# Kernel optimization log

Hardware: AMD Instinct MI355X
Metric: run time of the kernel (lower is better)

Reference implementation:

```python
import jax, jax.numpy as jnp
import numpy as np

C = 256
D = C // 8  # query/key channels


def setup_inputs() -> dict:
    key = jax.random.key(0)
    ks = jax.random.split(key, 7)
    x = jax.random.normal(ks[0], (4, C, 64, 64), dtype=jnp.float32)
    s1 = 1.0 / np.sqrt(C)
    w1 = jax.random.normal(ks[1], (D, C), dtype=jnp.float32) * s1
    b1 = jax.random.normal(ks[2], (D,), dtype=jnp.float32) * 0.01
    w2 = jax.random.normal(ks[3], (D, C), dtype=jnp.float32) * s1
    b2 = jax.random.normal(ks[4], (D,), dtype=jnp.float32) * 0.01
    w3 = jax.random.normal(ks[5], (C, C), dtype=jnp.float32) * s1
    b3 = jax.random.normal(ks[6], (C,), dtype=jnp.float32) * 0.01
    return {"x": x, "w1": w1, "b1": b1, "w2": w2, "b2": b2, "w3": w3, "b3": b3}


def reference(x, w1, b1, w2, b2, w3, b3):
    B, Cc, W, H = x.shape
    N = W * H
    xf = x.reshape(B, Cc, N)  # [B, C, N] flattened spatial
    # 1x1 convs are per-pixel linear maps over channels
    q = jnp.einsum('dc,bcn->bnd', w1, xf) + b1  # [B, N, D]
    k = jnp.einsum('dc,bcn->bdn', w2, xf) + b2[:, None]  # [B, D, N]
    v = jnp.einsum('oc,bcn->bon', w3, xf) + b3[:, None]  # [B, C, N]
    energy = jnp.einsum('bnd,bdm->bnm', q, k)  # [B, N, N]
    attn = jax.nn.softmax(energy, axis=-1)
    out = jnp.einsum('bcm,bnm->bcn', v, attn)  # bmm(V, attn^T)
    out = out.reshape(B, Cc, W, H) + x
    return out
```

## Files before the change

kernel.cpp:

```cpp
#include <hip/hip_runtime.h>
#include <hip/hip_fp16.h>

typedef _Float16 half8 __attribute__((ext_vector_type(8)));
typedef _Float16 half2v __attribute__((ext_vector_type(2)));
typedef float f32x16 __attribute__((ext_vector_type(16)));
typedef float f32x4v __attribute__((ext_vector_type(4)));

#define MFMA16(A, B, C) __builtin_amdgcn_mfma_f32_32x32x16_f16((A), (B), (C), 0, 0, 0)

__device__ __forceinline__ f32x16 fzero16() {
  f32x16 z;
#pragma unroll
  for (int i = 0; i < 16; ++i) z[i] = 0.0f;
  return z;
}

struct HiLo { _Float16 hi, lo; };
__device__ __forceinline__ HiLo split1(float f) {
  HiLo r;
  r.hi = (_Float16)f;
  r.lo = (_Float16)(f - (float)r.hi);
  return r;
}

__global__ __launch_bounds__(256) void wprep_kernel(
    const float* __restrict__ w1, const float* __restrict__ w2,
    const float* __restrict__ w3,
    _Float16* __restrict__ w1p, _Float16* __restrict__ w2p,
    _Float16* __restrict__ w3p)
{
  const int t = threadIdx.x;
  const int blk = blockIdx.x;
  if (blk < 8) {
    const int cot = blk;
    for (int e = t; e < 8192; e += 256) {
      const int j = e & 7, l = (e >> 3) & 63, cs = e >> 9;
      const int lr = l & 31, h = l >> 5;
      const int row = cot * 32 + lr;
      const int col = cs * 16 + 4 * h + (j & 3) + 8 * (j >> 2);
      const HiLo s = split1(w3[row * 256 + col]);
      const int idx = ((cot * 16 + cs) * 64 + l) * 8 + j;
      w3p[idx] = s.hi;
      w3p[65536 + idx] = s.lo;
    }
  } else {
    for (int e = t; e < 8192; e += 256) {
      const int j = e & 7, l = (e >> 3) & 63, cs = e >> 9;
      const int lr = l & 31, h = l >> 5;
      const int col = cs * 16 + 4 * h + (j & 3) + 8 * (j >> 2);
      const HiLo s1 = split1(w1[lr * 256 + col]);
      const HiLo s2 = split1(w2[lr * 256 + col]);
      const int idx = (cs * 64 + l) * 8 + j;
      w1p[idx] = s1.hi; w1p[8192 + idx] = s1.lo;
      w2p[idx] = s2.hi; w2p[8192 + idx] = s2.lo;
    }
  }
}

__global__ __launch_bounds__(256) void qk_proj_kernel(
    const float* __restrict__ x,
    const _Float16* __restrict__ w1p, const float* __restrict__ b1,
    const _Float16* __restrict__ w2p, const float* __restrict__ b2,
    _Float16* __restrict__ qb, _Float16* __restrict__ kb)
{
  __shared__ f32x4v red[4][2][4][64];
  const int t = threadIdx.x, w = t >> 6, l = t & 63;
  const int lr = l & 31, h = l >> 5;
  const int b = blockIdx.x >> 7;
  const int rt = blockIdx.x & 127;
  const float* xb = x + (size_t)b * 256 * 4096 + rt * 32 + lr;

  f32x16 accq = fzero16(), acck = fzero16();

  for (int cs = w * 4; cs < w * 4 + 4; ++cs) {
    const int c0 = cs * 16 + 4 * h;
    half8 xh, xl;
#pragma unroll
    for (int j = 0; j < 8; ++j) {
      const int c = c0 + (j & 3) + 8 * (j >> 2);
      const HiLo s = split1(xb[(size_t)c * 4096]);
      xh[j] = s.hi; xl[j] = s.lo;
    }
    const half8 w1h = *(const half8*)&w1p[(cs * 64 + l) * 8];
    const half8 w1l = *(const half8*)&w1p[8192 + (cs * 64 + l) * 8];
    const half8 w2h = *(const half8*)&w2p[(cs * 64 + l) * 8];
    const half8 w2l = *(const half8*)&w2p[8192 + (cs * 64 + l) * 8];
    accq = MFMA16(w1h, xh, accq);
    accq = MFMA16(w1h, xl, accq);
    accq = MFMA16(w1l, xh, accq);
    acck = MFMA16(w2h, xh, acck);
    acck = MFMA16(w2h, xl, acck);
    acck = MFMA16(w2l, xh, acck);
  }

#pragma unroll
  for (int i4 = 0; i4 < 4; ++i4) {
    f32x4v q4, k4;
#pragma unroll
    for (int c = 0; c < 4; ++c) { q4[c] = accq[4 * i4 + c]; k4[c] = acck[4 * i4 + c]; }
    red[w][0][i4][l] = q4;
    red[w][1][i4][l] = k4;
  }
  __syncthreads();
  if (w < 2) {
    _Float16* dst = (w == 0) ? qb : kb;
    const float* bias = (w == 0) ? b1 : b2;
    f32x16 tot;
#pragma unroll
    for (int i4 = 0; i4 < 4; ++i4) {
      f32x4v v = red[0][w][i4][l];
      v += red[1][w][i4][l];
      v += red[2][w][i4][l];
      v += red[3][w][i4][l];
#pragma unroll
      for (int c = 0; c < 4; ++c) tot[4 * i4 + c] = v[c];
    }
#pragma unroll
    for (int ds = 0; ds < 2; ++ds) {
      half8 ph;
#pragma unroll
      for (int j = 0; j < 8; ++j) {
        const int d = 16 * ds + 4 * h + (j & 3) + 8 * (j >> 2);
        ph[j] = (_Float16)(tot[8 * ds + j] + bias[d]);
      }
      *(half8*)&dst[((((size_t)b * 128 + rt) * 2 + ds) * 64 + l) * 8] = ph;
    }
  }
}

__global__ __launch_bounds__(256) void v_proj_kernel(
    const float* __restrict__ x, const _Float16* __restrict__ w3p,
    const float* __restrict__ b3, _Float16* __restrict__ vb)
{
  const int t = threadIdx.x, w = t >> 6, l = t & 63;
  const int lr = l & 31, h = l >> 5;
  const int b = blockIdx.x >> 7;
  const int nt = blockIdx.x & 127;
  const float* xb = x + (size_t)b * 256 * 4096 + nt * 32 + lr;
  const int cot0 = w * 2, cot1 = w * 2 + 1;

  f32x16 acc0 = fzero16(), acc1 = fzero16();

  for (int cs = 0; cs < 16; ++cs) {
    const int c0 = cs * 16 + 4 * h;
    half8 xh, xl;
#pragma unroll
    for (int j = 0; j < 8; ++j) {
      const int c = c0 + (j & 3) + 8 * (j >> 2);
      const HiLo s = split1(xb[(size_t)c * 4096]);
      xh[j] = s.hi; xl[j] = s.lo;
    }
    const half8 wh0 = *(const half8*)&w3p[((cot0 * 16 + cs) * 64 + l) * 8];
    const half8 wl0 = *(const half8*)&w3p[65536 + ((cot0 * 16 + cs) * 64 + l) * 8];
    const half8 wh1 = *(const half8*)&w3p[((cot1 * 16 + cs) * 64 + l) * 8];
    const half8 wl1 = *(const half8*)&w3p[65536 + ((cot1 * 16 + cs) * 64 + l) * 8];
    acc0 = MFMA16(xh, wh0, acc0);
    acc0 = MFMA16(xl, wh0, acc0);
    acc0 = MFMA16(xh, wl0, acc0);
    acc1 = MFMA16(xh, wh1, acc1);
    acc1 = MFMA16(xl, wh1, acc1);
    acc1 = MFMA16(xh, wl1, acc1);
  }

  const float bv0 = b3[cot0 * 32 + lr];
  const float bv1 = b3[cot1 * 32 + lr];
#pragma unroll
  for (int hfq = 0; hfq < 2; ++hfq) {
    half8 p0, p1;
#pragma unroll
    for (int j = 0; j < 8; ++j) {
      p0[j] = (_Float16)(acc0[8 * hfq + j] + bv0);
      p1[j] = (_Float16)(acc1[8 * hfq + j] + bv1);
    }
    const int ms = nt * 2 + hfq;
    *(half8*)&vb[((((size_t)b * 256 + ms) * 8 + cot0) * 64 + l) * 8] = p0;
    *(half8*)&vb[((((size_t)b * 256 + ms) * 8 + cot1) * 64 + l) * 8] = p1;
  }
}

__global__ __launch_bounds__(512) void rowmax_kernel(
    const _Float16* __restrict__ qb, const _Float16* __restrict__ kb,
    float* __restrict__ Mrow)
{
  __shared__ float red[2][8][32];
  const int t = threadIdx.x, w = t >> 6, l = t & 63;
  const int bid = blockIdx.x;
  const int xcd = bid & 7;
  const int b = xcd >> 1;
  const int sp = ((bid >> 3) << 1) | (xcd & 1);
  const int sl0 = sp * 2, sl1 = sp * 2 + 1;
  const _Float16* qp0 = qb + ((((size_t)b * 128 + sl0) * 2) * 64 + l) * 8;
  const _Float16* qp1 = qb + ((((size_t)b * 128 + sl1) * 2) * 64 + l) * 8;
  const half8 q00 = *(const half8*)qp0;
  const half8 q01 = *(const half8*)(qp0 + 512);
  const half8 q10 = *(const half8*)qp1;
  const half8 q11 = *(const half8*)(qp1 + 512);
  float vm0 = -3.0e38f, vm1 = -3.0e38f;
  for (int mt = w * 16; mt < w * 16 + 16; ++mt) {
    const _Float16* kp = kb + ((((size_t)b * 128 + mt) * 2) * 64 + l) * 8;
    const half8 k0 = *(const half8*)kp;
    const half8 k1 = *(const half8*)(kp + 512);
    f32x16 s0 = fzero16();
    s0 = MFMA16(k0, q00, s0);
    s0 = MFMA16(k1, q01, s0);
    f32x16 s1 = fzero16();
    s1 = MFMA16(k0, q10, s1);
    s1 = MFMA16(k1, q11, s1);
#pragma unroll
    for (int i = 0; i < 16; ++i) {
      vm0 = fmaxf(vm0, s0[i]);
      vm1 = fmaxf(vm1, s1[i]);
    }
  }
  vm0 = fmaxf(vm0, __shfl_xor(vm0, 32));
  vm1 = fmaxf(vm1, __shfl_xor(vm1, 32));
  if (l < 32) { red[0][w][l] = vm0; red[1][w][l] = vm1; }
  __syncthreads();
  if (t < 64) {
    const int slab = t >> 5, r = t & 31;
    float m = red[slab][0][r];
#pragma unroll
    for (int ww = 1; ww < 8; ++ww) m = fmaxf(m, red[slab][ww][r]);
    Mrow[(size_t)b * 4096 + (sp * 2 + slab) * 32 + r] = m;
  }
}

__global__ __launch_bounds__(512, 1) void attn_kernel(
    const _Float16* __restrict__ qb, const _Float16* __restrict__ kb,
    const _Float16* __restrict__ vb, const float* __restrict__ Mrow,
    const float* __restrict__ x, float* __restrict__ out)
{
  __shared__ __align__(16) _Float16 Plds[2][2][2][8][64][8];
  __shared__ float Lred[2][4][32];
  const int t = threadIdx.x, w = t >> 6, l = t & 63;
  const int lr = l & 31, h = l >> 5;
  const int bid = blockIdx.x;
  const int xcd = bid & 7;
  const int b = xcd >> 1;
  const int rg = ((bid >> 3) << 1) | (xcd & 1);
  const int sw = w >> 2;
  const int kq = w & 3;

  const _Float16* kbase = kb + (size_t)b * 131072 + (size_t)l * 8;
  const _Float16* vbase = vb + (size_t)b * 1048576 + (size_t)w * 512 + (size_t)l * 8;

#define KF(kt, ds) (*(const half8*)(kbase + ((size_t)(((kt) * 4 + kq) * 2 + (ds))) * 512))
#define VF(kt, ks) (*(const half8*)(vbase + ((size_t)(((kt) * 8 + (ks)) * 8)) * 512))

  const int rt32q = rg * 2 + sw;
  const _Float16* qp = qb + (((size_t)b * 128 + rt32q) * 2 * 64 + l) * 8;
  const half8 qf0 = *(const half8*)qp;
  const half8 qf1 = *(const half8*)(qp + 512);
  const float LOG2E = 1.44269504088896340736f;
  const float Mr = Mrow[(size_t)b * 4096 + rt32q * 32 + lr];
  const float nM2 = -Mr * LOG2E;

  f32x16 acc0 = fzero16(), acc1 = fzero16();
  float Lacc = 0.f;
  half8 va0[8], va1[8];
  half8 ka0, ka1, kb0_, kb1_;

#define EXPPACK(S, BUF, TI)                                                    \
  {                                                                            \
    float pvv[16];                                                             \
    float ls = 0.f;                                                            \
    _Pragma("unroll") for (int i = 0; i < 16; ++i) {                           \
      pvv[i] = exp2f(fmaf((S)[i], LOG2E, nM2)); ls += pvv[i];                  \
    }                                                                          \
    Lacc += ls;                                                                \
    union { half8 v; half2v h2[4]; } u0, u1;                                   \
    _Pragma("unroll") for (int jj = 0; jj < 4; ++jj) {                         \
      auto a0 = __builtin_amdgcn_cvt_pkrtz(pvv[2 * jj], pvv[2 * jj + 1]);      \
      auto a1 = __builtin_amdgcn_cvt_pkrtz(pvv[8 + 2 * jj], pvv[8 + 2 * jj + 1]); \
      u0.h2[jj] = *(half2v*)&a0;                                               \
      u1.h2[jj] = *(half2v*)&a1;                                               \
    }                                                                          \
    *(half8*)&Plds[BUF][TI][sw][kq * 2 + 0][l][0] = u0.v;                      \
    *(half8*)&Plds[BUF][TI][sw][kq * 2 + 1][l][0] = u1.v;                      \
  }

#define PVC(CB, TI, VA)                                                        \
  {                                                                            \
    __builtin_amdgcn_s_setprio(1);                                             \
    _Pragma("unroll") for (int ks = 0; ks < 8; ++ks) {                         \
      const half8 pb0 = *(const half8*)&Plds[CB][TI][0][ks][l][0];             \
      const half8 pb1 = *(const half8*)&Plds[CB][TI][1][ks][l][0];             \
      acc0 = MFMA16(VA[ks], pb0, acc0);                                        \
      acc1 = MFMA16(VA[ks], pb1, acc1);                                        \
    }                                                                          \
    __builtin_amdgcn_s_setprio(0);                                             \
  }

#pragma unroll
  for (int ks = 0; ks < 8; ++ks) va0[ks] = VF(0, ks);
#pragma unroll
  for (int ks = 0; ks < 8; ++ks) va1[ks] = VF(1, ks);
  {
    const half8 k00 = KF(0, 0), k01 = KF(0, 1);
    f32x16 s = fzero16();
    s = MFMA16(k00, qf0, s);
    s = MFMA16(k01, qf1, s);
    ka0 = KF(2, 0); ka1 = KF(2, 1);
    EXPPACK(s, 0, 0)
  }
  {
    const half8 k10 = KF(1, 0), k11 = KF(1, 1);
    f32x16 s = fzero16();
    s = MFMA16(k10, qf0, s);
    s = MFMA16(k11, qf1, s);
    kb0_ = KF(3, 0); kb1_ = KF(3, 1);
    EXPPACK(s, 0, 1)
  }
  asm volatile("s_waitcnt lgkmcnt(0)" ::: "memory");
  __builtin_amdgcn_s_barrier();
  asm volatile("" ::: "memory");

  for (int P = 0; P < 16; ++P) {
    const int CB = P & 1, PB = CB ^ 1;
    const int p0 = 2 * P + 2, p1 = 2 * P + 3;

    if (p0 < 32) {
      f32x16 s = fzero16();
      s = MFMA16(ka0, qf0, s);
      s = MFMA16(ka1, qf1, s);
      if (p0 + 2 < 32) { ka0 = KF(p0 + 2, 0); ka1 = KF(p0 + 2, 1); }
      EXPPACK(s, PB, 0)
    }
    PVC(CB, 0, va0)
    if (p0 < 32) {
#pragma unroll
      for (int ks = 0; ks < 8; ++ks) va0[ks] = VF(p0, ks);
    }

    if (p1 < 32) {
      f32x16 s = fzero16();
      s = MFMA16(kb0_, qf0, s);
      s = MFMA16(kb1_, qf1, s);
      if (p1 + 2 < 32) { kb0_ = KF(p1 + 2, 0); kb1_ = KF(p1 + 2, 1); }
      EXPPACK(s, PB, 1)
    }
    PVC(CB, 1, va1)
    if (p1 < 32) {
#pragma unroll
      for (int ks = 0; ks < 8; ++ks) va1[ks] = VF(p1, ks);
    }

    asm volatile("s_waitcnt lgkmcnt(0)" ::: "memory");
    __builtin_amdgcn_s_barrier();
    asm volatile("" ::: "memory");
  }
#undef PVC
#undef EXPPACK
#undef KF
#undef VF

  {
    const float l2 = Lacc + __shfl_xor(Lacc, 32);
    if (l < 32) Lred[sw][kq][lr] = l2;
  }
  __syncthreads();
  const float invL0 = 1.0f / (Lred[0][0][lr] + Lred[0][1][lr] + Lred[0][2][lr] + Lred[0][3][lr]);
  const float invL1 = 1.0f / (Lred[1][0][lr] + Lred[1][1][lr] + Lred[1][2][lr] + Lred[1][3][lr]);

  const float* xb = x + (size_t)b * 1048576;
  float* ob = out + (size_t)b * 1048576;
  const int nn0 = rg * 64 + lr;
  const int nn1 = rg * 64 + 32 + lr;
#pragma unroll
  for (int reg = 0; reg < 16; ++reg) {
    const int crel = (reg & 3) + 8 * (reg >> 2) + 4 * h;
    const int cout = w * 32 + crel;
    const size_t o0 = (size_t)cout * 4096 + nn0;
    ob[o0] = acc0[reg] * invL0 + xb[o0];
    const size_t o1 = (size_t)cout * 4096 + nn1;
    ob[o1] = acc1[reg] * invL1 + xb[o1];
  }
}

extern "C" void kernel_launch(void* const* d_in, const int* in_sizes, int n_in,
                              void* d_out, int out_size, void* d_ws, size_t ws_size,
                              hipStream_t stream) {
  const float* x  = (const float*)d_in[0];
  const float* w1 = (const float*)d_in[1];
  const float* b1 = (const float*)d_in[2];
  const float* w2 = (const float*)d_in[3];
  const float* b2 = (const float*)d_in[4];
  const float* w3 = (const float*)d_in[5];
  const float* b3 = (const float*)d_in[6];
  float* out = (float*)d_out;

  char* ws = (char*)d_ws;
  _Float16* qb  = (_Float16*)(ws);
  _Float16* kb  = (_Float16*)(ws + (1u << 20));
  _Float16* vb  = (_Float16*)(ws + (2u << 20));
  float*    Mrow = (float*)(ws + (10u << 20));
  _Float16* w1p = (_Float16*)(ws + (10u << 20) + (64u << 10));
  _Float16* w2p = (_Float16*)(ws + (10u << 20) + (96u << 10));
  _Float16* w3p = (_Float16*)(ws + (10u << 20) + (128u << 10));

  hipLaunchKernelGGL(wprep_kernel, dim3(9), dim3(256), 0, stream,
                     w1, w2, w3, w1p, w2p, w3p);
  hipLaunchKernelGGL(qk_proj_kernel, dim3(512), dim3(256), 0, stream,
                     x, w1p, b1, w2p, b2, qb, kb);
  hipLaunchKernelGGL(v_proj_kernel, dim3(512), dim3(256), 0, stream,
                     x, w3p, b3, vb);
  hipLaunchKernelGGL(rowmax_kernel, dim3(256), dim3(512), 0, stream, qb, kb, Mrow);
  hipLaunchKernelGGL(attn_kernel, dim3(256), dim3(512), 0, stream,
                     qb, kb, vb, Mrow, x, out);
}
```

Measured before the change: 87.86 us.

## Fuse QK and V projections, remap attention PV work per wave, tree rowmax

Merges the separate Q/K and V projection kernels into one kernel so x is read and split into fp16 hi/lo once instead of twice, and one launch is removed. In the attention kernel each wave now handles one query slab and two channel tiles instead of one channel tile across both slabs. This halves the P-fragment LDS reads per PV step but doubles the V registers held per wave. The rowmax kernel's serial max chain is replaced by a tree of three-way max ops to shorten the dependency chain. The added register pressure in attention may lower occupancy or cause spills.

```diff
diff --git a/kernel.cpp b/kernel.cpp
--- a/kernel.cpp
+++ b/kernel.cpp
@@ -2,7 +2,6 @@
 #include <hip/hip_fp16.h>
 
 typedef _Float16 half8 __attribute__((ext_vector_type(8)));
-typedef _Float16 half2v __attribute__((ext_vector_type(2)));
 typedef float f32x16 __attribute__((ext_vector_type(16)));
 typedef float f32x4v __attribute__((ext_vector_type(4)));
 
@@ -57,81 +56,15 @@
   }
 }
 
-__global__ __launch_bounds__(256) void qk_proj_kernel(
+__global__ __launch_bounds__(256) void qkv_proj_kernel(
     const float* __restrict__ x,
     const _Float16* __restrict__ w1p, const float* __restrict__ b1,
     const _Float16* __restrict__ w2p, const float* __restrict__ b2,
-    _Float16* __restrict__ qb, _Float16* __restrict__ kb)
+    const _Float16* __restrict__ w3p, const float* __restrict__ b3,
+    _Float16* __restrict__ qb, _Float16* __restrict__ kb,
+    _Float16* __restrict__ vb)
 {
   __shared__ f32x4v red[4][2][4][64];
-  const int t = threadIdx.x, w = t >> 6, l = t & 63;
-  const int lr = l & 31, h = l >> 5;
-  const int b = blockIdx.x >> 7;
-  const int rt = blockIdx.x & 127;
-  const float* xb = x + (size_t)b * 256 * 4096 + rt * 32 + lr;
-
-  f32x16 accq = fzero16(), acck = fzero16();
-
-  for (int cs = w * 4; cs < w * 4 + 4; ++cs) {
-    const int c0 = cs * 16 + 4 * h;
-    half8 xh, xl;
-#pragma unroll
-    for (int j = 0; j < 8; ++j) {
-      const int c = c0 + (j & 3) + 8 * (j >> 2);
-      const HiLo s = split1(xb[(size_t)c * 4096]);
-      xh[j] = s.hi; xl[j] = s.lo;
-    }
-    const half8 w1h = *(const half8*)&w1p[(cs * 64 + l) * 8];
-    const half8 w1l = *(const half8*)&w1p[8192 + (cs * 64 + l) * 8];
-    const half8 w2h = *(const half8*)&w2p[(cs * 64 + l) * 8];
-    const half8 w2l = *(const half8*)&w2p[8192 + (cs * 64 + l) * 8];
-    accq = MFMA16(w1h, xh, accq);
-    accq = MFMA16(w1h, xl, accq);
-    accq = MFMA16(w1l, xh, accq);
-    acck = MFMA16(w2h, xh, acck);
-    acck = MFMA16(w2h, xl, acck);
-    acck = MFMA16(w2l, xh, acck);
-  }
-
-#pragma unroll
-  for (int i4 = 0; i4 < 4; ++i4) {
-    f32x4v q4, k4;
-#pragma unroll
-    for (int c = 0; c < 4; ++c) { q4[c] = accq[4 * i4 + c]; k4[c] = acck[4 * i4 + c]; }
-    red[w][0][i4][l] = q4;
-    red[w][1][i4][l] = k4;
-  }
-  __syncthreads();
-  if (w < 2) {
-    _Float16* dst = (w == 0) ? qb : kb;
-    const float* bias = (w == 0) ? b1 : b2;
-    f32x16 tot;
-#pragma unroll
-    for (int i4 = 0; i4 < 4; ++i4) {
-      f32x4v v = red[0][w][i4][l];
-      v += red[1][w][i4][l];
-      v += red[2][w][i4][l];
-      v += red[3][w][i4][l];
-#pragma unroll
-      for (int c = 0; c < 4; ++c) tot[4 * i4 + c] = v[c];
-    }
-#pragma unroll
-    for (int ds = 0; ds < 2; ++ds) {
-      half8 ph;
-#pragma unroll
-      for (int j = 0; j < 8; ++j) {
-        const int d = 16 * ds + 4 * h + (j & 3) + 8 * (j >> 2);
-        ph[j] = (_Float16)(tot[8 * ds + j] + bias[d]);
-      }
-      *(half8*)&dst[((((size_t)b * 128 + rt) * 2 + ds) * 64 + l) * 8] = ph;
-    }
-  }
-}
-
-__global__ __launch_bounds__(256) void v_proj_kernel(
-    const float* __restrict__ x, const _Float16* __restrict__ w3p,
-    const float* __restrict__ b3, _Float16* __restrict__ vb)
-{
   const int t = threadIdx.x, w = t >> 6, l = t & 63;
   const int lr = l & 31, h = l >> 5;
   const int b = blockIdx.x >> 7;
@@ -139,7 +72,8 @@
   const float* xb = x + (size_t)b * 256 * 4096 + nt * 32 + lr;
   const int cot0 = w * 2, cot1 = w * 2 + 1;
 
-  f32x16 acc0 = fzero16(), acc1 = fzero16();
+  f32x16 accq = fzero16(), acck = fzero16();
+  f32x16 accv0 = fzero16(), accv1 = fzero16();
 
   for (int cs = 0; cs < 16; ++cs) {
     const int c0 = cs * 16 + 4 * h;
@@ -154,12 +88,24 @@
     const half8 wl0 = *(const half8*)&w3p[65536 + ((cot0 * 16 + cs) * 64 + l) * 8];
     const half8 wh1 = *(const half8*)&w3p[((cot1 * 16 + cs) * 64 + l) * 8];
     const half8 wl1 = *(const half8*)&w3p[65536 + ((cot1 * 16 + cs) * 64 + l) * 8];
-    acc0 = MFMA16(xh, wh0, acc0);
-    acc0 = MFMA16(xl, wh0, acc0);
-    acc0 = MFMA16(xh, wl0, acc0);
-    acc1 = MFMA16(xh, wh1, acc1);
-    acc1 = MFMA16(xl, wh1, acc1);
-    acc1 = MFMA16(xh, wl1, acc1);
+    accv0 = MFMA16(xh, wh0, accv0);
+    accv0 = MFMA16(xl, wh0, accv0);
+    accv0 = MFMA16(xh, wl0, accv0);
+    accv1 = MFMA16(xh, wh1, accv1);
+    accv1 = MFMA16(xl, wh1, accv1);
+    accv1 = MFMA16(xh, wl1, accv1);
+    if ((cs >> 2) == w) {
+      const half8 w1h = *(const half8*)&w1p[(cs * 64 + l) * 8];
+      const half8 w1l = *(const half8*)&w1p[8192 + (cs * 64 + l) * 8];
+      const half8 w2h = *(const half8*)&w2p[(cs * 64 + l) * 8];
+      const half8 w2l = *(const half8*)&w2p[8192 + (cs * 64 + l) * 8];
+      accq = MFMA16(w1h, xh, accq);
+      accq = MFMA16(w1h, xl, accq);
+      accq = MFMA16(w1l, xh, accq);
+      acck = MFMA16(w2h, xh, acck);
+      acck = MFMA16(w2h, xl, acck);
+      acck = MFMA16(w2l, xh, acck);
+    }
   }
 
   const float bv0 = b3[cot0 * 32 + lr];
@@ -169,13 +115,58 @@
     half8 p0, p1;
 #pragma unroll
     for (int j = 0; j < 8; ++j) {
-      p0[j] = (_Float16)(acc0[8 * hfq + j] + bv0);
-      p1[j] = (_Float16)(acc1[8 * hfq + j] + bv1);
+      p0[j] = (_Float16)(accv0[8 * hfq + j] + bv0);
+      p1[j] = (_Float16)(accv1[8 * hfq + j] + bv1);
     }
     const int ms = nt * 2 + hfq;
     *(half8*)&vb[((((size_t)b * 256 + ms) * 8 + cot0) * 64 + l) * 8] = p0;
     *(half8*)&vb[((((size_t)b * 256 + ms) * 8 + cot1) * 64 + l) * 8] = p1;
   }
+
+#pragma unroll
+  for (int i4 = 0; i4 < 4; ++i4) {
+    f32x4v q4, k4;
+#pragma unroll
+    for (int c = 0; c < 4; ++c) { q4[c] = accq[4 * i4 + c]; k4[c] = acck[4 * i4 + c]; }
+    red[w][0][i4][l] = q4;
+    red[w][1][i4][l] = k4;
+  }
+  __syncthreads();
+  if (w < 2) {
+    _Float16* dst = (w == 0) ? qb : kb;
+    const float* bias = (w == 0) ? b1 : b2;
+    f32x16 tot;
+#pragma unroll
+    for (int i4 = 0; i4 < 4; ++i4) {
+      f32x4v v = red[0][w][i4][l];
+      v += red[1][w][i4][l];
+      v += red[2][w][i4][l];
+      v += red[3][w][i4][l];
+#pragma unroll
+      for (int c = 0; c < 4; ++c) tot[4 * i4 + c] = v[c];
+    }
+#pragma unroll
+    for (int ds = 0; ds < 2; ++ds) {
+      half8 ph;
+#pragma unroll
+      for (int j = 0; j < 8; ++j) {
+        const int d = 16 * ds + 4 * h + (j & 3) + 8 * (j >> 2);
+        ph[j] = (_Float16)(tot[8 * ds + j] + bias[d]);
+      }
+      *(half8*)&dst[((((size_t)b * 128 + nt) * 2 + ds) * 64 + l) * 8] = ph;
+    }
+  }
+}
+
+__device__ __forceinline__ float max16(float vm, const f32x16& s) {
+  const float g1 = fmaxf(fmaxf(s[0], s[1]), s[2]);
+  const float g2 = fmaxf(fmaxf(s[3], s[4]), s[5]);
+  const float g3 = fmaxf(fmaxf(s[6], s[7]), s[8]);
+  const float g4 = fmaxf(fmaxf(s[9], s[10]), s[11]);
+  const float g5 = fmaxf(fmaxf(s[12], s[13]), s[14]);
+  const float h1 = fmaxf(fmaxf(g1, g2), g3);
+  const float h2 = fmaxf(fmaxf(g4, g5), s[15]);
+  return fmaxf(fmaxf(vm, h1), h2);
 }
 
 __global__ __launch_bounds__(512) void rowmax_kernel(
@@ -206,11 +197,8 @@
     f32x16 s1 = fzero16();
     s1 = MFMA16(k0, q10, s1);
     s1 = MFMA16(k1, q11, s1);
-#pragma unroll
-    for (int i = 0; i < 16; ++i) {
-      vm0 = fmaxf(vm0, s0[i]);
-      vm1 = fmaxf(vm1, s1[i]);
-    }
+    vm0 = max16(vm0, s0);
+    vm1 = max16(vm1, s1);
   }
   vm0 = fmaxf(vm0, __shfl_xor(vm0, 32));
   vm1 = fmaxf(vm1, __shfl_xor(vm1, 32));
@@ -240,12 +228,13 @@
   const int rg = ((bid >> 3) << 1) | (xcd & 1);
   const int sw = w >> 2;
   const int kq = w & 3;
+  const int cg = w & 3;
 
   const _Float16* kbase = kb + (size_t)b * 131072 + (size_t)l * 8;
-  const _Float16* vbase = vb + (size_t)b * 1048576 + (size_t)w * 512 + (size_t)l * 8;
+  const _Float16* vbase = vb + (size_t)b * 1048576 + (size_t)(cg * 2) * 512 + (size_t)l * 8;
 
 #define KF(kt, ds) (*(const half8*)(kbase + ((size_t)(((kt) * 4 + kq) * 2 + (ds))) * 512))
-#define VF(kt, ks) (*(const half8*)(vbase + ((size_t)(((kt) * 8 + (ks)) * 8)) * 512))
+#define VF(kt, ks, ci) (*(const half8*)(vbase + ((size_t)(((kt) * 8 + (ks)) * 8 + (ci))) * 512))
 
   const int rt32q = rg * 2 + sw;
   const _Float16* qp = qb + (((size_t)b * 128 + rt32q) * 2 * 64 + l) * 8;
@@ -257,7 +246,7 @@
 
   f32x16 acc0 = fzero16(), acc1 = fzero16();
   float Lacc = 0.f;
-  half8 va0[8], va1[8];
+  half8 va0[16], va1[16];
   half8 ka0, ka1, kb0_, kb1_;
 
 #define EXPPACK(S, BUF, TI)                                                    \
@@ -268,33 +257,32 @@
       pvv[i] = exp2f(fmaf((S)[i], LOG2E, nM2)); ls += pvv[i];                  \
     }                                                                          \
     Lacc += ls;                                                                \
-    union { half8 v; half2v h2[4]; } u0, u1;                                   \
+    half8 ph0, ph1;                                                            \
     _Pragma("unroll") for (int jj = 0; jj < 4; ++jj) {                         \
       auto a0 = __builtin_amdgcn_cvt_pkrtz(pvv[2 * jj], pvv[2 * jj + 1]);      \
       auto a1 = __builtin_amdgcn_cvt_pkrtz(pvv[8 + 2 * jj], pvv[8 + 2 * jj + 1]); \
-      u0.h2[jj] = *(half2v*)&a0;                                               \
-      u1.h2[jj] = *(half2v*)&a1;                                               \
+      ph0[2 * jj] = a0[0]; ph0[2 * jj + 1] = a0[1];                            \
+      ph1[2 * jj] = a1[0]; ph1[2 * jj + 1] = a1[1];                            \
     }                                                                          \
-    *(half8*)&Plds[BUF][TI][sw][kq * 2 + 0][l][0] = u0.v;                      \
-    *(half8*)&Plds[BUF][TI][sw][kq * 2 + 1][l][0] = u1.v;                      \
+    *(half8*)&Plds[BUF][TI][sw][kq * 2 + 0][l][0] = ph0;                       \
+    *(half8*)&Plds[BUF][TI][sw][kq * 2 + 1][l][0] = ph1;                       \
   }
 
 #define PVC(CB, TI, VA)                                                        \
   {                                                                            \
     __builtin_amdgcn_s_setprio(1);                                             \
     _Pragma("unroll") for (int ks = 0; ks < 8; ++ks) {                         \
-      const half8 pb0 = *(const half8*)&Plds[CB][TI][0][ks][l][0];             \
-      const half8 pb1 = *(const half8*)&Plds[CB][TI][1][ks][l][0];             \
-      acc0 = MFMA16(VA[ks], pb0, acc0);                                        \
-      acc1 = MFMA16(VA[ks], pb1, acc1);                                        \
+      const half8 pb = *(const half8*)&Plds[CB][TI][sw][ks][l][0];             \
+      acc0 = MFMA16(VA[ks], pb, acc0);                                         \
+      acc1 = MFMA16(VA[8 + ks], pb, acc1);                                     \
     }                                                                          \
     __builtin_amdgcn_s_setprio(0);                                             \
   }
 
 #pragma unroll
-  for (int ks = 0; ks < 8; ++ks) va0[ks] = VF(0, ks);
-#pragma unroll
-  for (int ks = 0; ks < 8; ++ks) va1[ks] = VF(1, ks);
+  for (int ks = 0; ks < 8; ++ks) { va0[ks] = VF(0, ks, 0); va0[8 + ks] = VF(0, ks, 1); }
+#pragma unroll
+  for (int ks = 0; ks < 8; ++ks) { va1[ks] = VF(1, ks, 0); va1[8 + ks] = VF(1, ks, 1); }
   {
     const half8 k00 = KF(0, 0), k01 = KF(0, 1);
     f32x16 s = fzero16();
@@ -329,7 +317,7 @@
     PVC(CB, 0, va0)
     if (p0 < 32) {
 #pragma unroll
-      for (int ks = 0; ks < 8; ++ks) va0[ks] = VF(p0, ks);
+      for (int ks = 0; ks < 8; ++ks) { va0[ks] = VF(p0, ks, 0); va0[8 + ks] = VF(p0, ks, 1); }
     }
 
     if (p1 < 32) {
@@ -342,7 +330,7 @@
     PVC(CB, 1, va1)
     if (p1 < 32) {
 #pragma unroll
-      for (int ks = 0; ks < 8; ++ks) va1[ks] = VF(p1, ks);
+      for (int ks = 0; ks < 8; ++ks) { va1[ks] = VF(p1, ks, 0); va1[8 + ks] = VF(p1, ks, 1); }
     }
 
     asm volatile("s_waitcnt lgkmcnt(0)" ::: "memory");
@@ -359,21 +347,18 @@
     if (l < 32) Lred[sw][kq][lr] = l2;
   }
   __syncthreads();
-  const float invL0 = 1.0f / (Lred[0][0][lr] + Lred[0][1][lr] + Lred[0][2][lr] + Lred[0][3][lr]);
-  const float invL1 = 1.0f / (Lred[1][0][lr] + Lred[1][1][lr] + Lred[1][2][lr] + Lred[1][3][lr]);
+  const float invL = 1.0f / (Lred[sw][0][lr] + Lred[sw][1][lr] + Lred[sw][2][lr] + Lred[sw][3][lr]);
 
   const float* xb = x + (size_t)b * 1048576;
   float* ob = out + (size_t)b * 1048576;
-  const int nn0 = rg * 64 + lr;
-  const int nn1 = rg * 64 + 32 + lr;
+  const int nn = rg * 64 + sw * 32 + lr;
 #pragma unroll
   for (int reg = 0; reg < 16; ++reg) {
     const int crel = (reg & 3) + 8 * (reg >> 2) + 4 * h;
-    const int cout = w * 32 + crel;
-    const size_t o0 = (size_t)cout * 4096 + nn0;
-    ob[o0] = acc0[reg] * invL0 + xb[o0];
-    const size_t o1 = (size_t)cout * 4096 + nn1;
-    ob[o1] = acc1[reg] * invL1 + xb[o1];
+    const size_t o0 = (size_t)((cg * 2 + 0) * 32 + crel) * 4096 + nn;
+    ob[o0] = acc0[reg] * invL + xb[o0];
+    const size_t o1 = (size_t)((cg * 2 + 1) * 32 + crel) * 4096 + nn;
+    ob[o1] = acc1[reg] * invL + xb[o1];
   }
 }
 
@@ -400,10 +385,8 @@
 
   hipLaunchKernelGGL(wprep_kernel, dim3(9), dim3(256), 0, stream,
                      w1, w2, w3, w1p, w2p, w3p);
-  hipLaunchKernelGGL(qk_proj_kernel, dim3(512), dim3(256), 0, stream,
-                     x, w1p, b1, w2p, b2, qb, kb);
-  hipLaunchKernelGGL(v_proj_kernel, dim3(512), dim3(256), 0, stream,
-                     x, w3p, b3, vb);
+  hipLaunchKernelGGL(qkv_proj_kernel, dim3(512), dim3(256), 0, stream,
+                     x, w1p, b1, w2p, b2, w3p, b3, qb, kb, vb);
   hipLaunchKernelGGL(rowmax_kernel, dim3(256), dim3(512), 0, stream, qb, kb, Mrow);
   hipLaunchKernelGGL(attn_kernel, dim3(256), dim3(512), 0, stream,
                      qb, kb, vb, Mrow, x, out);
```

Measured after the change: 96.16 us. 1.09x slower.
